# Performance work log

Hardware: AMD Instinct MI355X
Metric: run time of the kernel (lower is better)

Reference implementation:

```python
import jax, jax.numpy as jnp
import numpy as np
from jax import lax

HEADS = 8
LN_EPS = 1e-5


def setup_inputs() -> dict:
    key = jax.random.key(0)
    k = jax.random.split(key, 8)
    B, C, H, W, r = 4, 64, 64, 64, 4
    T = H * W
    x = jax.random.normal(k[0], (B, C, H, W), dtype=jnp.float32)
    conv_w = jax.random.normal(k[1], (C, C, r, r), dtype=jnp.float32) * 0.02  # OIHW
    conv_b = jnp.zeros((C,), dtype=jnp.float32)
    ln_g = jnp.ones((C,), dtype=jnp.float32)
    ln_b = jnp.zeros((C,), dtype=jnp.float32)
    Wqkv = jax.random.normal(k[2], (C, 3 * C), dtype=jnp.float32) * 0.02  # to_qvk (no bias)
    W0 = jax.random.normal(k[3], (C, C), dtype=jnp.float32) * 0.02  # output proj (no bias)
    E = jax.random.normal(k[4], (T, T // 4), dtype=jnp.float32)  # Linformer proj (randn in torch fwd)
    return {"x": x, "conv_w": conv_w, "conv_b": conv_b, "ln_g": ln_g,
            "ln_b": ln_b, "Wqkv": Wqkv, "W0": W0, "E": E}


def _layernorm2d(y, g, b):
    # LayerNorm over channel dim of NCHW (torch: permute to NHWC, LN last dim)
    yt = y.transpose(0, 2, 3, 1)  # b h w c
    mu = yt.mean(-1, keepdims=True)
    var = ((yt - mu) ** 2).mean(-1, keepdims=True)
    yt = (yt - mu) * lax.rsqrt(var + LN_EPS) * g + b
    return yt.transpose(0, 3, 1, 2)


def reference(x, conv_w, conv_b, ln_g, ln_b, Wqkv, W0, E):
    B, C, H, W = x.shape
    T = H * W
    dh = C // HEADS
    r = conv_w.shape[-1]

    # reducer: conv(stride=r) + LayerNorm2d. NOTE: faithful to the torch module,
    # this result is computed but NEVER used by the output (dead code in source).
    red = lax.conv_general_dilated(x, conv_w, (r, r), 'VALID',
                                   dimension_numbers=('NCHW', 'OIHW', 'NCHW'))
    red = red + conv_b[None, :, None, None]
    _red = _layernorm2d(red, ln_g, ln_b)  # unused, matches source

    # tokens from full-resolution x: b c h w -> b (h w) c
    xf = x.reshape(B, C, T).transpose(0, 2, 1)  # [B,T,C]
    qkv = xf @ Wqkv  # [B,T,3C]
    # rearrange 'b t (d k h)' with k=3, h=HEADS -> composite order (d, k, h)
    qkv = qkv.reshape(B, T, dh, 3, HEADS)
    q = qkv[:, :, :, 0, :].transpose(0, 3, 1, 2)  # [B,h,T,d]
    kk = qkv[:, :, :, 1, :].transpose(0, 3, 1, 2)
    v = qkv[:, :, :, 2, :].transpose(0, 3, 1, 2)

    # Linformer low-rank projection of V and K: [B,h,T,d] x [T,k] -> [B,h,k,d]
    v = jnp.einsum('bhjd,jk->bhkd', v, E)
    kk = jnp.einsum('bhjd,jk->bhkd', kk, E)

    scale = dh ** -0.5
    scores = jnp.einsum('bhid,bhjd->bhij', q, kk) * scale  # [B,h,T,k]
    attn = jax.nn.softmax(scores, axis=-1)
    out = jnp.einsum('bhij,bhjd->bhid', attn, v)  # [B,h,T,d]

    out = out.transpose(0, 2, 1, 3).reshape(B, T, C)  # b h i d -> b i (h d)
    out = out @ W0  # [B,T,C]
    return out.transpose(0, 2, 1).reshape(B, C, H, W)
```

## Files before the change

### kernel.cpp

```cpp
#include <hip/hip_runtime.h>

#define T_DIM 4096
#define KD    1024
#define SCALE 0.35355339059327373f

typedef __attribute__((ext_vector_type(8))) short bf16x8;
typedef __attribute__((ext_vector_type(4))) short bf16x4;
typedef __attribute__((ext_vector_type(4))) float f32x4;

__device__ inline unsigned short f2bf(float f) {
  unsigned u = __float_as_uint(f);
  unsigned r = u + 0x7fffu + ((u >> 16) & 1u);
  return (unsigned short)(r >> 16);
}

__device__ inline unsigned cvt_pk_bf16(float a, float b) {
  unsigned ua = __float_as_uint(a); ua += 0x7fffu + ((ua >> 16) & 1u);
  unsigned ub = __float_as_uint(b); ub += 0x7fffu + ((ub >> 16) & 1u);
  return (ua >> 16) | (ub & 0xffff0000u);
}

__device__ inline unsigned pk_trunc(float a, float b) {
  return (__float_as_uint(a) >> 16) | (__float_as_uint(b) & 0xffff0000u);
}

__device__ inline bf16x4 mk4(unsigned lo, unsigned hi) {
  union { unsigned u[2]; bf16x4 v; } x; x.u[0] = lo; x.u[1] = hi; return x.v;
}

__device__ inline bf16x8 mk8(unsigned a, unsigned b, unsigned c, unsigned d) {
  union { unsigned u[4]; bf16x8 v; } x;
  x.u[0] = a; x.u[1] = b; x.u[2] = c; x.u[3] = d; return x.v;
}

__device__ inline f32x4 mfma16(bf16x4 a, bf16x4 b, f32x4 c) {
  bf16x8 a8 = {}, b8 = {};
  a8[0] = a[0]; a8[1] = a[1]; a8[2] = a[2]; a8[3] = a[3];
  b8[0] = b[0]; b8[1] = b[1]; b8[2] = b[2]; b8[3] = b[3];
  return __builtin_amdgcn_mfma_f32_16x16x32_bf16(a8, b8, c, 0, 0, 0);
}

__global__ __launch_bounds__(256) void k_front(const float* __restrict__ x,
                                               const float* __restrict__ E,
                                               const float* __restrict__ Wqkv,
                                               float* __restrict__ partial,
                                               float* __restrict__ Q) {
  const int bid = blockIdx.x;
  const int tid = threadIdx.x;

  if (bid < 512) {
    const int kb = bid & 7;
    const int b  = (bid >> 3) & 3;
    const int s  = bid >> 5;
    const int k0 = kb * 128;
    const int lane = tid & 63;
    const int w = tid >> 6;
    const int li = lane & 15, lg = lane >> 4;

    f32x4 acc[4][2] = {};
#pragma unroll 2
    for (int tb = 0; tb < 8; ++tb) {
      const int tbase = s * 256 + tb * 32 + lg * 8;
      bf16x8 bq[2];
#pragma unroll
      for (int nt = 0; nt < 2; ++nt) {
        const int kcol = k0 + w * 32 + nt * 16 + li;
        float bv[8];
#pragma unroll
        for (int j = 0; j < 8; ++j)
          bv[j] = E[(size_t)(tbase + j) * KD + kcol];
        bq[nt] = mk8(cvt_pk_bf16(bv[0], bv[1]), cvt_pk_bf16(bv[2], bv[3]),
                     cvt_pk_bf16(bv[4], bv[5]), cvt_pk_bf16(bv[6], bv[7]));
      }
#pragma unroll
      for (int mt = 0; mt < 4; ++mt) {
        const float* ap = x + ((size_t)b * 64 + mt * 16 + li) * T_DIM + tbase;
        float4 a0 = *(const float4*)(ap);
        float4 a1 = *(const float4*)(ap + 4);
        bf16x8 af8 = mk8(cvt_pk_bf16(a0.x, a0.y), cvt_pk_bf16(a0.z, a0.w),
                         cvt_pk_bf16(a1.x, a1.y), cvt_pk_bf16(a1.z, a1.w));
        acc[mt][0] = __builtin_amdgcn_mfma_f32_16x16x32_bf16(af8, bq[0], acc[mt][0], 0, 0, 0);
        acc[mt][1] = __builtin_amdgcn_mfma_f32_16x16x32_bf16(af8, bq[1], acc[mt][1], 0, 0, 0);
      }
    }
    float* pb = partial + ((size_t)s * 4 + b) * (64 * KD);
#pragma unroll
    for (int mt = 0; mt < 4; ++mt)
#pragma unroll
      for (int nt = 0; nt < 2; ++nt) {
        const int row = mt * 16 + lg * 4;
        const int col = k0 + w * 32 + nt * 16 + li;
#pragma unroll
        for (int reg = 0; reg < 4; ++reg)
          pb[(size_t)(row + reg) * KD + col] = acc[mt][nt][reg];
      }
  } else {
    const int idx = bid - 512;
    const int g  = idx & 7;
    const int tt = (idx >> 3) & 15;
    const int b  = idx >> 7;
    const int t  = tt * 256 + tid;
    const int col0 = g * 24;

    float acc[8];
#pragma unroll
    for (int j = 0; j < 8; ++j) acc[j] = 0.f;
    const float* xb = x + (size_t)b * 64 * T_DIM + t;
#pragma unroll 4
    for (int c = 0; c < 64; ++c) {
      float xv = xb[(size_t)c * T_DIM];
      const float* wr = Wqkv + c * 192 + col0;
#pragma unroll
      for (int h = 0; h < 8; ++h) acc[h] += xv * wr[h];
    }
#pragma unroll
    for (int h = 0; h < 8; ++h)
      Q[(((size_t)(b * 8 + h)) * 8 + g) * T_DIM + t] = acc[h];
  }
}

__global__ __launch_bounds__(256) void k_xkv(const float* __restrict__ partial,
                                             const float* __restrict__ Wqkv,
                                             uint2* __restrict__ Kg,
                                             unsigned short* __restrict__ Vg) {
  __shared__ unsigned short XPs[64 * 72];
  const int kb = blockIdx.x;
  const int h  = blockIdx.y;
  const int b  = blockIdx.z;
  const int tid = threadIdx.x;

  {
    const int kk = tid & 63;
    const int cg = tid >> 6;
#pragma unroll
    for (int u = 0; u < 16; ++u) {
      const int c = cg * 16 + u;
      const size_t src = (size_t)c * KD + kb * 64 + kk;
      float a = 0.f;
#pragma unroll
      for (int s = 0; s < 16; ++s)
        a += partial[((size_t)s * 4 + b) * (64 * KD) + src];
      XPs[c * 72 + kk] = f2bf(a);
    }
  }
  __syncthreads();

  const int klocal = tid & 63;
  const int sel    = (tid >> 6) & 1;
  const int dg     = tid >> 7;
  const int k      = kb * 64 + klocal;

  float acc[4];
#pragma unroll
  for (int d = 0; d < 4; ++d) acc[d] = 0.f;
#pragma unroll 4
  for (int c = 0; c < 64; ++c) {
    float xv = __uint_as_float((unsigned)XPs[c * 72 + klocal] << 16);
    const float* wr = Wqkv + c * 192 + (sel + 1) * 8 + h;
#pragma unroll
    for (int d = 0; d < 4; ++d) acc[d] += xv * wr[(dg * 4 + d) * 24];
  }

  const int bh = b * 8 + h;
  if (sel == 0) {
    uint2* kg = Kg + (size_t)bh * 2048;
    kg[dg * 1024 + k] = make_uint2(cvt_pk_bf16(acc[0] * SCALE, acc[1] * SCALE),
                                   cvt_pk_bf16(acc[2] * SCALE, acc[3] * SCALE));
  } else {
#pragma unroll
    for (int d = 0; d < 4; ++d)
      Vg[(size_t)(bh * 8 + dg * 4 + d) * KD + k] = f2bf(acc[d]);
  }
}

#define VT_PITCH 1032
__global__ __launch_bounds__(256) void k_attn(const float* __restrict__ Q,
                                              const uint2* __restrict__ Kg,
                                              const unsigned short* __restrict__ Vg,
                                              unsigned short* __restrict__ Ob) {
  __shared__ unsigned short Kt[2 * 1024 * 4];
  __shared__ unsigned short Vt[9 * VT_PITCH];
  const int bh = blockIdx.x;
  const int tid = threadIdx.x;

  const uint2* kg = Kg + (size_t)bh * 2048;
  uint2* kt2 = (uint2*)Kt;
#pragma unroll
  for (int it = 0; it < 8; ++it)
    kt2[it * 256 + tid] = kg[it * 256 + tid];
  const unsigned* vg = (const unsigned*)(Vg + (size_t)bh * 8192);
#pragma unroll
  for (int dd = 0; dd < 8; ++dd) {
#pragma unroll
    for (int it = 0; it < 2; ++it) {
      const int j2 = it * 256 + tid;
      *(unsigned*)(Vt + dd * VT_PITCH + j2 * 2) = vg[dd * 512 + j2];
    }
  }
#pragma unroll
  for (int it = 0; it < 2; ++it)
    *(unsigned*)(Vt + 8 * VT_PITCH + (it * 256 + tid) * 2) = 0x3F803F80u;
  __syncthreads();

  const int lane = tid & 63, w = tid >> 6;
  const int li = lane & 15, lg = lane >> 4;
  const int i0w = blockIdx.y * 128 + w * 32;

  bf16x4 qf[2] = {bf16x4{}, bf16x4{}};
  if (lane < 32) {
#pragma unroll
    for (int it2 = 0; it2 < 2; ++it2) {
      const float* qp = Q + ((size_t)bh * 8 + lg * 4) * T_DIM + i0w + it2 * 16 + li;
      qf[it2] = mk4(cvt_pk_bf16(qp[0], qp[T_DIM]),
                    cvt_pk_bf16(qp[2 * T_DIM], qp[3 * T_DIM]));
    }
  }

  f32x4 accO[2] = {f32x4{0.f, 0.f, 0.f, 0.f}, f32x4{0.f, 0.f, 0.f, 0.f}};
#pragma unroll 2
  for (int jt = 0; jt < 1024; jt += 16) {
    bf16x4 kf = {};
    if (lane < 32) kf = *(const bf16x4*)(&Kt[(size_t)(lg * 1024 + jt + li) * 4]);
    bf16x4 vf = {};
    if (li < 9) vf = *(const bf16x4*)(&Vt[li * VT_PITCH + jt + lg * 4]);
#pragma unroll
    for (int it2 = 0; it2 < 2; ++it2) {
      f32x4 st = mfma16(kf, qf[it2], f32x4{0.f, 0.f, 0.f, 0.f});
      f32x4 p;
      p[0] = __expf(st[0]); p[1] = __expf(st[1]);
      p[2] = __expf(st[2]); p[3] = __expf(st[3]);
      bf16x4 pf = mk4(pk_trunc(p[0], p[1]), pk_trunc(p[2], p[3]));
      accO[it2] = mfma16(vf, pf, accO[it2]);
    }
  }

  const int b = bh >> 3, h = bh & 7;
#pragma unroll
  for (int it2 = 0; it2 < 2; ++it2) {
    float l = __shfl(accO[it2][0], 32 + li);
    float inv = 1.0f / l;
    if (lane < 32) {
      const int i = i0w + it2 * 16 + li;
      unsigned p0 = cvt_pk_bf16(accO[it2][0] * inv, accO[it2][1] * inv);
      unsigned p1 = cvt_pk_bf16(accO[it2][2] * inv, accO[it2][3] * inv);
      *(uint2*)(Ob + ((size_t)b * T_DIM + i) * 64 + h * 8 + lg * 4) =
          make_uint2(p0, p1);
    }
  }
}

__global__ __launch_bounds__(256) void k_out(const unsigned short* __restrict__ Ob,
                                             const float* __restrict__ W0,
                                             float* __restrict__ out) {
  const int cg_ = blockIdx.x;
  const int tt = blockIdx.y;
  const int b  = blockIdx.z;
  const int t  = tt * 256 + threadIdx.x;
  const int col0 = cg_ * 8;

  float acc[8];
#pragma unroll
  for (int j = 0; j < 8; ++j) acc[j] = 0.f;
  const unsigned short* orow = Ob + ((size_t)b * T_DIM + t) * 64;
#pragma unroll
  for (int c0 = 0; c0 < 64; c0 += 4) {
    uint2 v = *(const uint2*)(orow + c0);
    float ov[4];
    ov[0] = __uint_as_float(v.x << 16);
    ov[1] = __uint_as_float(v.x & 0xffff0000u);
    ov[2] = __uint_as_float(v.y << 16);
    ov[3] = __uint_as_float(v.y & 0xffff0000u);
#pragma unroll
    for (int u = 0; u < 4; ++u) {
      const float* wr = W0 + (c0 + u) * 64 + col0;
#pragma unroll
      for (int j = 0; j < 8; ++j) acc[j] += ov[u] * wr[j];
    }
  }
#pragma unroll
  for (int j = 0; j < 8; ++j)
    out[((size_t)b * 64 + col0 + j) * T_DIM + t] = acc[j];
}

extern "C" void kernel_launch(void* const* d_in, const int* in_sizes, int n_in,
                              void* d_out, int out_size, void* d_ws, size_t ws_size,
                              hipStream_t stream) {
  const float* x    = (const float*)d_in[0];
  const float* Wqkv = (const float*)d_in[5];
  const float* W0   = (const float*)d_in[6];
  const float* E    = (const float*)d_in[7];
  float* out = (float*)d_out;

  float* Q           = (float*)d_ws;
  float* partial     = Q + 1048576;
  unsigned short* Ob = (unsigned short*)(partial + 4194304);
  uint2* Kg          = (uint2*)(Ob + 1048576);
  unsigned short* Vg = (unsigned short*)(Kg + 65536);

  k_front <<<dim3(1024),     256, 0, stream>>>(x, E, Wqkv, partial, Q);
  k_xkv   <<<dim3(16, 8, 4), 256, 0, stream>>>(partial, Wqkv, Kg, Vg);
  k_attn  <<<dim3(32, 32),   256, 0, stream>>>(Q, Kg, Vg, Ob);
  k_out   <<<dim3(8, 16, 4), 256, 0, stream>>>(Ob, W0, out);
}
```

Measured before the change: 152.6 us.

## Restructure k_xkv grid so each block reduces partials once for all heads

Changes the k_xkv decomposition from one block per (k-block of 64, head, batch) to one block per (k-block of 16, batch, K-or-V). Each block sums the 16 split-K partials for its 16 keys once and reuses them across all 8 heads. Before, every head's block re-read and re-reduced the same partial slice. This removes the 8x redundant global reads of the partial buffer, at the cost of two reductions (one per K/V selector) and narrower 32-bit K stores that keep the same memory layout.

```diff
diff --git a/kernel.cpp b/kernel.cpp
--- a/kernel.cpp
+++ b/kernel.cpp
@@ -121,55 +121,56 @@
 
 __global__ __launch_bounds__(256) void k_xkv(const float* __restrict__ partial,
                                              const float* __restrict__ Wqkv,
-                                             uint2* __restrict__ Kg,
+                                             unsigned* __restrict__ Kg32,
                                              unsigned short* __restrict__ Vg) {
-  __shared__ unsigned short XPs[64 * 72];
-  const int kb = blockIdx.x;
-  const int h  = blockIdx.y;
-  const int b  = blockIdx.z;
+  __shared__ unsigned short XPs[64 * 16];
+  const int kb  = blockIdx.x;
+  const int b   = blockIdx.y;
+  const int sel = blockIdx.z;
   const int tid = threadIdx.x;
+  const int k0 = kb * 16;
 
   {
-    const int kk = tid & 63;
-    const int cg = tid >> 6;
-#pragma unroll
-    for (int u = 0; u < 16; ++u) {
-      const int c = cg * 16 + u;
-      const size_t src = (size_t)c * KD + kb * 64 + kk;
+    const int kk = tid & 15;
+    const int cq = tid >> 4;
+#pragma unroll
+    for (int u = 0; u < 4; ++u) {
+      const int c = cq * 4 + u;
+      const size_t src = (size_t)c * KD + k0 + kk;
       float a = 0.f;
 #pragma unroll
       for (int s = 0; s < 16; ++s)
         a += partial[((size_t)s * 4 + b) * (64 * KD) + src];
-      XPs[c * 72 + kk] = f2bf(a);
+      XPs[c * 16 + kk] = f2bf(a);
     }
   }
   __syncthreads();
 
-  const int klocal = tid & 63;
-  const int sel    = (tid >> 6) & 1;
-  const int dg     = tid >> 7;
-  const int k      = kb * 64 + klocal;
-
-  float acc[4];
-#pragma unroll
-  for (int d = 0; d < 4; ++d) acc[d] = 0.f;
+  const int w = tid >> 6;
+  const int lane = tid & 63;
+  const int kk = lane & 15;
+  const int dg = lane >> 4;
+  const int k  = k0 + kk;
+
+#pragma unroll
+  for (int cc = 0; cc < 2; ++cc) {
+    const int h = w * 2 + cc;
+    float a0 = 0.f, a1 = 0.f;
 #pragma unroll 4
-  for (int c = 0; c < 64; ++c) {
-    float xv = __uint_as_float((unsigned)XPs[c * 72 + klocal] << 16);
-    const float* wr = Wqkv + c * 192 + (sel + 1) * 8 + h;
-#pragma unroll
-    for (int d = 0; d < 4; ++d) acc[d] += xv * wr[(dg * 4 + d) * 24];
-  }
-
-  const int bh = b * 8 + h;
-  if (sel == 0) {
-    uint2* kg = Kg + (size_t)bh * 2048;
-    kg[dg * 1024 + k] = make_uint2(cvt_pk_bf16(acc[0] * SCALE, acc[1] * SCALE),
-                                   cvt_pk_bf16(acc[2] * SCALE, acc[3] * SCALE));
-  } else {
-#pragma unroll
-    for (int d = 0; d < 4; ++d)
-      Vg[(size_t)(bh * 8 + dg * 4 + d) * KD + k] = f2bf(acc[d]);
+    for (int c = 0; c < 64; ++c) {
+      float xv = __uint_as_float((unsigned)XPs[c * 16 + kk] << 16);
+      const float* wr = Wqkv + c * 192 + (sel + 1) * 8 + h;
+      a0 += xv * wr[(dg * 2 + 0) * 24];
+      a1 += xv * wr[(dg * 2 + 1) * 24];
+    }
+    const int bh = b * 8 + h;
+    if (sel == 0) {
+      unsigned pk = cvt_pk_bf16(a0 * SCALE, a1 * SCALE);
+      Kg32[(size_t)bh * 4096 + (dg >> 1) * 2048 + k * 2 + (dg & 1)] = pk;
+    } else {
+      Vg[(size_t)(bh * 8 + dg * 2 + 0) * KD + k] = f2bf(a0);
+      Vg[(size_t)(bh * 8 + dg * 2 + 1) * KD + k] = f2bf(a1);
+    }
   }
 }
 
@@ -298,7 +299,7 @@
   unsigned short* Vg = (unsigned short*)(Kg + 65536);
 
   k_front <<<dim3(1024),     256, 0, stream>>>(x, E, Wqkv, partial, Q);
-  k_xkv   <<<dim3(16, 8, 4), 256, 0, stream>>>(partial, Wqkv, Kg, Vg);
+  k_xkv   <<<dim3(64, 4, 2), 256, 0, stream>>>(partial, Wqkv, (unsigned*)Kg, Vg);
   k_attn  <<<dim3(32, 32),   256, 0, stream>>>(Q, Kg, Vg, Ob);
   k_out   <<<dim3(8, 16, 4), 256, 0, stream>>>(Ob, W0, out);
 }
```

After: 154.2 us. About the same (+1.1%).
